# Optimization experiments

Measured on AMD Instinct MI355X. Metric: run time of the kernel, lower is better.

The kernel has to match this reference:

```python
import jax, jax.numpy as jnp
import numpy as np

B, S, D = 2, 1024, 512
NH, HD = 8, 64          # num_heads, head_dim
NS, F3 = 8, 1536        # shared experts, ffn_dim_shared = 3*D
E, F2 = 32, 1024        # routed experts, ffn_dim_routed = 2*D
R, K = 64, 4            # router_rank, num_activated_experts


def _ln(x, w, b, eps=1e-5):
    m = x.mean(-1, keepdims=True)
    v = ((x - m) ** 2).mean(-1, keepdims=True)
    return (x - m) * jax.lax.rsqrt(v + eps) * w + b


def _rms(x, w, eps=1e-6):
    return x * jax.lax.rsqrt((x * x).mean(-1, keepdims=True) + eps) * w


def _l2n(x, eps=1e-12):
    return x / jnp.maximum(jnp.linalg.norm(x, axis=-1, keepdims=True), eps)


def setup_inputs() -> dict:
    key = jax.random.key(0)
    ks = iter(jax.random.split(key, 40))
    sc = 0.02
    n = lambda shape: jax.random.normal(next(ks), shape, dtype=jnp.float32) * sc
    inp = {
        'x': jax.random.normal(next(ks), (B, S, D), dtype=jnp.float32),
        'ln1_w': jnp.ones((D,)), 'ln1_b': jnp.zeros((D,)),
        'ln2_w': jnp.ones((D,)), 'ln2_b': jnp.zeros((D,)),
        # per-head attention params, stacked over heads
        'q_w': n((NH, D, HD)), 'q_b': jnp.zeros((NH, HD)),
        'k_w': n((NH, D, HD)), 'k_b': jnp.zeros((NH, HD)),
        'v_w': n((NH, D, HD)), 'v_b': jnp.zeros((NH, HD)),
        'aw1': n((NH, D, HD // 2)), 'ab1': jnp.zeros((NH, HD // 2)),
        'aw2': n((NH, HD // 2, HD)), 'ab2': jnp.zeros((NH, HD)),
        'bw': n((NH, D, HD)), 'bb': jnp.zeros((NH, HD)),
        'scw1': n((NH, D, HD // 2)), 'scb1': jnp.zeros((NH, HD // 2)),
        'scw2': n((NH, HD // 2, HD)), 'scb2': jnp.zeros((NH, HD)),
        'arms_w': jnp.ones((NH, HD)),
        'l1_w': n((NH, HD, HD)), 'l1_b': jnp.zeros((NH, HD)),
        'out_w': n((D, D)), 'out_b': jnp.zeros((D,)),
        # MoE params
        'sh_rms': jnp.ones((NS, D)),
        'sh_w1': n((NS, D, F3)), 'sh_w2': n((NS, F3, D)), 'sh_w3': n((NS, D, F3)),
        'r_w1': n((E, D, F2)), 'r_w2': n((E, F2, D)), 'r_w3': n((E, D, F2)),
        'rd_w': n((D, R)), 'ru_w': n((R, E)),
    }
    return inp


def _forward(x, ln1_w, ln1_b, ln2_w, ln2_b, q_w, q_b, k_w, k_b, v_w, v_b,
             aw1, ab1, aw2, ab2, bw, bb, scw1, scb1, scw2, scb2, arms_w,
             l1_w, l1_b, out_w, out_b, sh_rms, sh_w1, sh_w2, sh_w3,
             r_w1, r_w2, r_w3, rd_w, ru_w):
    silu, sig = jax.nn.silu, jax.nn.sigmoid
    # ---- attention sublayer (dropout = identity in eval) ----
    residual = x
    xn = _ln(x, ln1_w, ln1_b)                                   # [B,S,D]
    q = _l2n(silu(jnp.einsum('bsd,hdk->bhsk', xn, q_w) + q_b[None, :, None, :]))
    k = _l2n(silu(jnp.einsum('bsd,hdk->bhsk', xn, k_w) + k_b[None, :, None, :]))
    v = silu(jnp.einsum('bsd,hdk->bhsk', xn, v_w) + v_b[None, :, None, :])
    alpha = sig(jnp.einsum('bhsr,hrk->bhsk',
                           jnp.einsum('bsd,hdr->bhsr', xn, aw1) + ab1[None, :, None, :],
                           aw2) + ab2[None, :, None, :])
    beta = sig(jnp.einsum('bsd,hdk->bhsk', xn, bw) + bb[None, :, None, :])
    shortcut = sig(jnp.einsum('bhsr,hrk->bhsk',
                              jnp.einsum('bsd,hdr->bhsr', xn, scw1) + scb1[None, :, None, :],
                              scw2) + scb2[None, :, None, :])
    v = v * alpha + beta
    scores = jnp.einsum('bhsk,bhtk->bhst', q, k) / jnp.sqrt(jnp.float32(HD))
    o = jnp.einsum('bhst,bhtk->bhsk', jax.nn.softmax(scores, axis=-1), v)
    o = _rms(o, arms_w[None, :, None, :]) * shortcut
    o = jnp.einsum('bhsk,hkj->bhsj', o, l1_w) + l1_b[None, :, None, :]
    o = o.transpose(0, 2, 1, 3).reshape(B, S, D)                # concat heads
    x = residual + (o @ out_w + out_b)
    # ---- MoE sublayer ----
    residual = x
    xf = _ln(x, ln2_w, ln2_b).reshape(-1, D)                    # [T,D]
    T = xf.shape[0]
    # shared experts (AdvancedExpert: rmsnorm -> swiglu -> +residual), averaged
    rb = xf * jax.lax.rsqrt((xf * xf).mean(-1, keepdims=True) + 1e-6)
    hn = rb[None] * sh_rms[:, None, :]                          # [NS,T,D]
    gate = silu(jnp.einsum('ntd,ndf->ntf', hn, sh_w1))
    val = jnp.einsum('ntd,ndf->ntf', hn, sh_w3)
    sh_out = jnp.einsum('ntf,nfd->ntd', gate * val, sh_w2) + xf[None]
    shared = sh_out.sum(0) / NS
    # router (low-rank) + top-k softmax weights
    logits = (xf @ rd_w) @ ru_w                                 # [T,E]
    top_v, top_i = jax.lax.top_k(logits, K)
    rw = jax.nn.softmax(top_v, axis=-1)                         # [T,K]
    w_full = jnp.zeros((T, E), xf.dtype).at[jnp.arange(T)[:, None], top_i].add(rw)
    # routed experts: dense compute, masked combine (same math)
    rg = silu(jnp.einsum('td,edf->etf', xf, r_w1))
    rv = jnp.einsum('td,edf->etf', xf, r_w3)
    eo = jnp.einsum('etf,efd->etd', rg * rv, r_w2)              # [E,T,D]
    routed = jnp.einsum('etd,te->td', eo, w_full)
    x = residual + (shared + routed).reshape(B, S, D)
    counts = jnp.zeros((E,), jnp.float32).at[top_i.reshape(-1)].add(1.0)
    load_balance_loss = jnp.var(counts, ddof=1)
    return x, load_balance_loss


def reference(x, ln1_w, ln1_b, ln2_w, ln2_b, q_w, q_b, k_w, k_b, v_w, v_b,
              aw1, ab1, aw2, ab2, bw, bb, scw1, scb1, scw2, scb2, arms_w,
              l1_w, l1_b, out_w, out_b, sh_rms, sh_w1, sh_w2, sh_w3,
              r_w1, r_w2, r_w3, rd_w, ru_w):
    return _forward(x, ln1_w, ln1_b, ln2_w, ln2_b, q_w, q_b, k_w, k_b, v_w, v_b,
                    aw1, ab1, aw2, ab2, bw, bb, scw1, scb1, scw2, scb2, arms_w,
                    l1_w, l1_b, out_w, out_b, sh_rms, sh_w1, sh_w2, sh_w3,
                    r_w1, r_w2, r_w3, rd_w, ru_w)
```

## Files before the change

kernel.cpp:

```cpp
#include <hip/hip_runtime.h>
#include <cmath>
#include <cstdint>


typedef __bf16 bf16;
typedef __bf16 bf16x8 __attribute__((ext_vector_type(8)));
typedef __bf16 bf16x4 __attribute__((ext_vector_type(4)));
typedef float  f32x4  __attribute__((ext_vector_type(4)));

static constexpr int Bb = 2, Ss = 1024, Dd = 512, NHh = 8, HDd = 64;
static constexpr int Tt = Bb * Ss;
static constexpr int NSs = 8, F3f = 1536;
static constexpr int Ee = 32, F2f = 1024;
static constexpr int SLOTCAP = 10240;
static constexpr int MAXTILE = 160;

__device__ inline float wavesum(float v) {
#pragma unroll
  for (int i = 1; i < 64; i <<= 1) v += __shfl_xor(v, i, 64);
  return v;
}
__device__ inline float blocksum(float v, float* sm) {
  v = wavesum(v);
  int wv = threadIdx.x >> 6;
// ... 96 lines not shown
    for (int r = 0; r < 4; ++r) {
      int grow = bm * 64 + wave * 16 + quad * 4 + r;
      float v;
      if (DUAL) {
        v = silu_f(acc0[nt][r]) * acc1[nt][r];
      } else {
        v = acc0[nt][r] * scale;
        if (bias) v += (float)bias[z * biasBatch + gcol];
        if (ACT == 1) v = silu_f(v);
        else if (ACT == 2) v = sigm_f(v);
      }
      if (RESID) v += (float)resid[(long)grow * resLd + gcol];
      long ci = (long)z * cBatch + (long)grow * ldc + gcol;
      if (ACCUM) atomicAdd((float*)Cv + ci, v);
      else if (OUTBF) ((bf16*)Cv)[ci] = (bf16)v;
      else ((float*)Cv)[ci] = v;
    }
  }
}

template <typename TI, int WANT, int SCALE>
__global__ __launch_bounds__(256) void tconv_k(
    const unsigned short* __restrict__ xdet,
    const TI* __restrict__ W, long wBatch,
    const TI* __restrict__ sc, long sBatch,
    bf16* __restrict__ Wt, long oBatch, int K, int N) {
  if (is_f32(xdet) != WANT) return;
  __shared__ float sT[64][65];
  const int tid = threadIdx.x;
  const int k0 = blockIdx.x * 64, n0 = blockIdx.y * 64, z = blockIdx.z;
  const TI* Wz = W + (long)z * wBatch;
  const int rr = tid >> 4, cc = (tid & 15) * 4;
#pragma unroll
  for (int it = 0; it < 4; ++it) {
    int row = it * 16 + rr;
    const TI* p = Wz + (long)(k0 + row) * N + n0 + cc;
    float v0, v1, v2, v3;
    if constexpr (sizeof(TI) == 4) {
      float4 v = *(const float4*)p;
      v0 = v.x; v1 = v.y; v2 = v.z; v3 = v.w;
    } else {
      bf16x4 v = *(const bf16x4*)p;
      v0 = (float)v[0]; v1 = (float)v[1]; v2 = (float)v[2]; v3 = (float)v[3];
    }
    if (SCALE) {
      float s = (float)sc[(long)z * sBatch + k0 + row];
      v0 *= s; v1 *= s; v2 *= s; v3 *= s;
    }
    sT[row][cc + 0] = v0; sT[row][cc + 1] = v1;
    sT[row][cc + 2] = v2; sT[row][cc + 3] = v3;
  }
  __syncthreads();
  bf16* Oz = Wt + (long)z * oBatch;
#pragma unroll
  for (int it = 0; it < 4; ++it) {
    int n = it * 16 + rr;
    bf16x4 ov;
#pragma unroll
    for (int j = 0; j < 4; ++j) ov[j] = (bf16)sT[cc + j][n];
    *(bf16x4*)(Oz + (long)(n0 + n) * K + k0 + cc) = ov;
  }
}

template <int DUAL, int ACCUM>
__global__ __launch_bounds__(256) void gemmT_k(
    const bf16* __restrict__ A, long aBatch, int lda,
    const bf16* __restrict__ B0t, const bf16* __restrict__ B1t, long bBatch,
    void* __restrict__ Cv, long cBatch, int ldc, int K, float scale) {
  __shared__ __align__(16) bf16 sA[128 * 40];
  __shared__ __align__(16) bf16 sB0[64 * 40];
  __shared__ __align__(16) bf16 sB1[DUAL ? 64 * 40 : 16];
  const int tid = threadIdx.x, wave = tid >> 6, lane = tid & 63;
  const int fm = lane & 15, quad = lane >> 4;
  const bf16* Az = A + (long)blockIdx.z * aBatch + (long)(blockIdx.x * 128) * lda;
  const bf16* B0z = B0t + (long)blockIdx.z * bBatch + (long)(blockIdx.y * 64) * K;
  const bf16* B1z = DUAL ? (B1t + (long)blockIdx.z * bBatch + (long)(blockIdx.y * 64) * K) : nullptr;
  f32x4 acc0[2][4], acc1[2][4];
  const f32x4 vz = {0.f, 0.f, 0.f, 0.f};
#pragma unroll
  for (int m = 0; m < 2; ++m)
#pragma unroll
    for (int n = 0; n < 4; ++n) { acc0[m][n] = vz; acc1[m][n] = vz; }
  const int srow = tid >> 2, sk0 = (tid & 3) * 8;
  for (int kb = 0; kb < K; kb += 32) {
    *(bf16x8*)(sA + srow * 40 + sk0) =
        *(const bf16x8*)(Az + (long)srow * lda + kb + sk0);
    *(bf16x8*)(sA + (srow + 64) * 40 + sk0) =
        *(const bf16x8*)(Az + (long)(srow + 64) * lda + kb + sk0);
    *(bf16x8*)(sB0 + srow * 40 + sk0) =
        *(const bf16x8*)(B0z + (long)srow * K + kb + sk0);
    if (DUAL)
      *(bf16x8*)(sB1 + srow * 40 + sk0) =
          *(const bf16x8*)(B1z + (long)srow * K + kb + sk0);
    __syncthreads();
    bf16x8 af0 = *(const bf16x8*)(sA + (wave * 32 + fm) * 40 + quad * 8);
    bf16x8 af1 = *(const bf16x8*)(sA + (wave * 32 + 16 + fm) * 40 + quad * 8);
#pragma unroll
    for (int nt = 0; nt < 4; ++nt) {
      bf16x8 b0 = *(const bf16x8*)(sB0 + (nt * 16 + fm) * 40 + quad * 8);
      acc0[0][nt] = __builtin_amdgcn_mfma_f32_16x16x32_bf16(af0, b0, acc0[0][nt], 0, 0, 0);
      acc0[1][nt] = __builtin_amdgcn_mfma_f32_16x16x32_bf16(af1, b0, acc0[1][nt], 0, 0, 0);
      if (DUAL) {
        bf16x8 b1 = *(const bf16x8*)(sB1 + (nt * 16 + fm) * 40 + quad * 8);
        acc1[0][nt] = __builtin_amdgcn_mfma_f32_16x16x32_bf16(af0, b1, acc1[0][nt], 0, 0, 0);
        acc1[1][nt] = __builtin_amdgcn_mfma_f32_16x16x32_bf16(af1, b1, acc1[1][nt], 0, 0, 0);
      }
    }
    __syncthreads();
  }
#pragma unroll
  for (int mt = 0; mt < 2; ++mt)
#pragma unroll
    for (int nt = 0; nt < 4; ++nt) {
      int col = blockIdx.y * 64 + nt * 16 + fm;
#pragma unroll
      for (int r = 0; r < 4; ++r) {
        int row = blockIdx.x * 128 + wave * 32 + mt * 16 + quad * 4 + r;
        long ci = (long)blockIdx.z * cBatch + (long)row * ldc + col;
        if (DUAL) {
          ((bf16*)Cv)[ci] = (bf16)(silu_f(acc0[mt][nt][r]) * acc1[mt][nt][r]);
        } else {
          float v = acc0[mt][nt][r] * scale;
          if (ACCUM) atomicAdd((float*)Cv + ci, v);
          else ((bf16*)Cv)[ci] = (bf16)v;
        }
      }
    }
}

__global__ __launch_bounds__(256) void moeT1_k(
    const int* __restrict__ tileExp, const int* __restrict__ tileStart,
    const int* __restrict__ slotTok, const bf16* __restrict__ xfb,
    const bf16* __restrict__ W1t, const bf16* __restrict__ W3t,
    bf16* __restrict__ hid) {
  int e = tileExp[blockIdx.x];
  if (e < 0) return;
  int slot0 = tileStart[blockIdx.x];
  __shared__ int sTok[64];
  __shared__ __align__(16) bf16 sA[64 * 40];
  __shared__ __align__(16) bf16 sB0[128 * 40];
  __shared__ __align__(16) bf16 sB1[128 * 40];
  const int tid = threadIdx.x, wave = tid >> 6, lane = tid & 63;
  const int fm = lane & 15, quad = lane >> 4;
  const int wr = wave >> 1, wc = wave & 1;
  if (tid < 64) sTok[tid] = slotTok[slot0 + tid];
  __syncthreads();
  const bf16* B0 = W1t + (long)e * (F2f * 512) + (long)(blockIdx.y * 128) * 512;
  const bf16* B1 = W3t + (long)e * (F2f * 512) + (long)(blockIdx.y * 128) * 512;
  f32x4 acc0[2][4], acc1[2][4];
  const f32x4 vz = {0.f, 0.f, 0.f, 0.f};
#pragma unroll
  for (int m = 0; m < 2; ++m)
#pragma unroll
    for (int n = 0; n < 4; ++n) { acc0[m][n] = vz; acc1[m][n] = vz; }
  const int srow = tid >> 2, sk0 = (tid & 3) * 8;
  const long atok = (long)sTok[srow] * 512;
  for (int kb = 0; kb < 512; kb += 32) {
    *(bf16x8*)(sA + srow * 40 + sk0) = *(const bf16x8*)(xfb + atok + kb + sk0);
    *(bf16x8*)(sB0 + srow * 40 + sk0) =
        *(const bf16x8*)(B0 + (long)srow * 512 + kb + sk0);
    *(bf16x8*)(sB0 + (srow + 64) * 40 + sk0) =
        *(const bf16x8*)(B0 + (long)(srow + 64) * 512 + kb + sk0);
    *(bf16x8*)(sB1 + srow * 40 + sk0) =
        *(const bf16x8*)(B1 + (long)srow * 512 + kb + sk0);
    *(bf16x8*)(sB1 + (srow + 64) * 40 + sk0) =
        *(const bf16x8*)(B1 + (long)(srow + 64) * 512 + kb + sk0);
    __syncthreads();
    bf16x8 af0 = *(const bf16x8*)(sA + (wr * 32 + fm) * 40 + quad * 8);
    bf16x8 af1 = *(const bf16x8*)(sA + (wr * 32 + 16 + fm) * 40 + quad * 8);
#pragma unroll
    for (int nt = 0; nt < 4; ++nt) {
      bf16x8 b0 = *(const bf16x8*)(sB0 + (wc * 64 + nt * 16 + fm) * 40 + quad * 8);
      acc0[0][nt] = __builtin_amdgcn_mfma_f32_16x16x32_bf16(af0, b0, acc0[0][nt], 0, 0, 0);
      acc0[1][nt] = __builtin_amdgcn_mfma_f32_16x16x32_bf16(af1, b0, acc0[1][nt], 0, 0, 0);
      bf16x8 b1 = *(const bf16x8*)(sB1 + (wc * 64 + nt * 16 + fm) * 40 + quad * 8);
      acc1[0][nt] = __builtin_amdgcn_mfma_f32_16x16x32_bf16(af0, b1, acc1[0][nt], 0, 0, 0);
      acc1[1][nt] = __builtin_amdgcn_mfma_f32_16x16x32_bf16(af1, b1, acc1[1][nt], 0, 0, 0);
    }
    __syncthreads();
  }
#pragma unroll
  for (int mt = 0; mt < 2; ++mt)
#pragma unroll
    for (int nt = 0; nt < 4; ++nt) {
      int col = blockIdx.y * 128 + wc * 64 + nt * 16 + fm;
#pragma unroll
      for (int r = 0; r < 4; ++r) {
        int row = wr * 32 + mt * 16 + quad * 4 + r;
        hid[(long)(slot0 + row) * F2f + col] =
            (bf16)(silu_f(acc0[mt][nt][r]) * acc1[mt][nt][r]);
      }
    }
}

__global__ __launch_bounds__(256) void moeT2_k(
    const int* __restrict__ tileExp, const int* __restrict__ tileStart,
    const int* __restrict__ slotTok, const float* __restrict__ slotW,
    const bf16* __restrict__ hid, const bf16* __restrict__ W2t,
    float* __restrict__ acc) {
  int e = tileExp[blockIdx.x];
  if (e < 0) return;
  int slot0 = tileStart[blockIdx.x];
  __shared__ int sTok[64];
  __shared__ float sW[64];
  __shared__ __align__(16) bf16 sA[64 * 40];
  __shared__ __align__(16) bf16 sB[128 * 40];
  const int tid = threadIdx.x, wave = tid >> 6, lane = tid & 63;
  const int fm = lane & 15, quad = lane >> 4;
  const int wr = wave >> 1, wc = wave & 1;
  if (tid < 64) { sTok[tid] = slotTok[slot0 + tid]; sW[tid] = slotW[slot0 + tid]; }
  __syncthreads();
  const bf16* B = W2t + (long)e * (512 * F2f) + (long)(blockIdx.y * 128) * F2f;
  f32x4 acc0[2][4];
  const f32x4 vz = {0.f, 0.f, 0.f, 0.f};
#pragma unroll
  for (int m = 0; m < 2; ++m)
#pragma unroll
    for (int n = 0; n < 4; ++n) acc0[m][n] = vz;
  const int srow = tid >> 2, sk0 = (tid & 3) * 8;
  for (int kb = 0; kb < F2f; kb += 32) {
    *(bf16x8*)(sA + srow * 40 + sk0) =
        *(const bf16x8*)(hid + (long)(slot0 + srow) * F2f + kb + sk0);
    *(bf16x8*)(sB + srow * 40 + sk0) =
        *(const bf16x8*)(B + (long)srow * F2f + kb + sk0);
    *(bf16x8*)(sB + (srow + 64) * 40 + sk0) =
        *(const bf16x8*)(B + (long)(srow + 64) * F2f + kb + sk0);
    __syncthreads();
    bf16x8 af0 = *(const bf16x8*)(sA + (wr * 32 + fm) * 40 + quad * 8);
    bf16x8 af1 = *(const bf16x8*)(sA + (wr * 32 + 16 + fm) * 40 + quad * 8);
#pragma unroll
    for (int nt = 0; nt < 4; ++nt) {
      bf16x8 b0 = *(const bf16x8*)(sB + (wc * 64 + nt * 16 + fm) * 40 + quad * 8);
      acc0[0][nt] = __builtin_amdgcn_mfma_f32_16x16x32_bf16(af0, b0, acc0[0][nt], 0, 0, 0);
      acc0[1][nt] = __builtin_amdgcn_mfma_f32_16x16x32_bf16(af1, b0, acc0[1][nt], 0, 0, 0);
    }
    __syncthreads();
  }
#pragma unroll
  for (int mt = 0; mt < 2; ++mt)
#pragma unroll
    for (int nt = 0; nt < 4; ++nt) {
      int col = blockIdx.y * 128 + wc * 64 + nt * 16 + fm;
#pragma unroll
      for (int r = 0; r < 4; ++r) {
        int row = wr * 32 + mt * 16 + quad * 4 + r;
        atomicAdd(acc + (long)sTok[row] * 512 + col, acc0[mt][nt][r] * sW[row]);
      }
    }
}

template <typename TB, int WANT>
__global__ __launch_bounds__(256) void moe1_k(
    const unsigned short* __restrict__ xdet,
    const int* __restrict__ tileExp, const int* __restrict__ tileStart,
    const int* __restrict__ slotTok,
    const bf16* __restrict__ xfb,
    const TB* __restrict__ W1, const TB* __restrict__ W3,
    bf16* __restrict__ hid, int Ps, int colOff, int Np) {
  if (is_f32(xdet) != WANT) return;
  int e = tileExp[blockIdx.x];
  if (e < 0) return;
  int slot0 = tileStart[blockIdx.x];
  __shared__ int sTok[64];
  __shared__ __align__(16) bf16 sA[64 * 40];
  __shared__ __align__(16) bf16 sB0[64 * 40];
  __shared__ __align__(16) bf16 sB1[64 * 40];
  const int tid = threadIdx.x;
  const int wave = tid >> 6, lane = tid & 63;
  const int fm = lane & 15, quad = lane >> 4;
  if (tid < 64) sTok[tid] = slotTok[slot0 + tid];
  __syncthreads();
  const TB* B0 = W1 + (long)e * 512 * F2f + colOff;
  const TB* B1 = W3 + (long)e * 512 * F2f + colOff;
  const int bn = blockIdx.y;
  f32x4 acc0[4], acc1[4];
  const f32x4 vz = {0.f, 0.f, 0.f, 0.f};
#pragma unroll
  for (int i = 0; i < 4; ++i) { acc0[i] = vz; acc1[i] = vz; }
  const int arow = tid >> 2, ak0 = (tid & 3) * 8;
  const int gn = bn * 64 + lane;
  const int wch = wave * 8;
  for (int kb = 0; kb < 512; kb += 32) {
    int tok = sTok[arow];
    *(bf16x8*)(sA + arow * 40 + ak0) =
        *(const bf16x8*)(xfb + (long)tok * 512 + kb + ak0);
    bf16x8 bv, cv;
    if (gn < Np) {
      const TB* bp = B0 + (long)(kb + wch) * F2f + gn;
      const TB* cp = B1 + (long)(kb + wch) * F2f + gn;
#pragma unroll
      for (int j = 0; j < 8; ++j) {
        bv[j] = (bf16)(float)bp[(long)j * F2f];
        cv[j] = (bf16)(float)cp[(long)j * F2f];
      }
    } else {
#pragma unroll
      for (int j = 0; j < 8; ++j) { bv[j] = (bf16)0.f; cv[j] = (bf16)0.f; }
    }
    *(bf16x8*)(sB0 + lane * 40 + wch) = bv;
    *(bf16x8*)(sB1 + lane * 40 + wch) = cv;
    __syncthreads();
    bf16x8 af = *(const bf16x8*)(sA + (wave * 16 + fm) * 40 + quad * 8);
#pragma unroll
    for (int nt = 0; nt < 4; ++nt) {
      bf16x8 bfr = *(const bf16x8*)(sB0 + (nt * 16 + fm) * 40 + quad * 8);
      acc0[nt] = __builtin_amdgcn_mfma_f32_16x16x32_bf16(af, bfr, acc0[nt], 0, 0, 0);
      bf16x8 bg = *(const bf16x8*)(sB1 + (nt * 16 + fm) * 40 + quad * 8);
      acc1[nt] = __builtin_amdgcn_mfma_f32_16x16x32_bf16(af, bg, acc1[nt], 0, 0, 0);
    }
    __syncthreads();
  }
#pragma unroll
  for (int nt = 0; nt < 4; ++nt) {
    int gcol = bn * 64 + nt * 16 + fm;
    if (gcol >= Np) continue;
#pragma unroll
    for (int r = 0; r < 4; ++r) {
      int row = wave * 16 + quad * 4 + r;
      hid[(long)(slot0 + row) * Ps + gcol] =
          (bf16)(silu_f(acc0[nt][r]) * acc1[nt][r]);
    }
  }
}

template <typename TB, int WANT>
__global__ __launch_bounds__(256) void moe2_k(
    const unsigned short* __restrict__ xdet,
    const int* __restrict__ tileExp, const int* __restrict__ tileStart,
    const int* __restrict__ slotTok, const float* __restrict__ slotW,
// ... 234 lines not shown
  float ms = wavesum(ov * ov) * (1.f / 64.f);
  float s = rsqrtf(ms + 1e-6f);
  o[i] = (bf16)(ov * s * (float)arms[h * 64 + lane] * (float)sc[i]);
}

template <typename T, int WANT>
__global__ __launch_bounds__(256) void router_k(const unsigned short* __restrict__ xdet,
                                                const float* __restrict__ x2,
                                                const T* __restrict__ lnw,
                                                const T* __restrict__ lnb,
                                                const T* __restrict__ rdw,
                                                const T* __restrict__ ruw,
                                                int* __restrict__ eidx,
                                                float* __restrict__ ew,
                                                int* __restrict__ counts) {
  if (is_f32(xdet) != WANT) return;
  __shared__ float sx[4][512];
  __shared__ float st[4][64];
  __shared__ float sl[4][32];
  int wv = threadIdx.x >> 6, lane = threadIdx.x & 63;
  long t = (long)blockIdx.x * 4 + wv;
  float v[8];
  float s1 = 0.f;
#pragma unroll
  for (int j = 0; j < 8; ++j) { v[j] = x2[t * 512 + lane * 8 + j]; s1 += v[j]; }
  float mean = wavesum(s1) * (1.f / 512.f);
  float s2 = 0.f;
#pragma unroll
  for (int j = 0; j < 8; ++j) { float d = v[j] - mean; s2 += d * d; }
  float rv = rsqrtf(wavesum(s2) * (1.f / 512.f) + 1e-5f);
#pragma unroll
  for (int j = 0; j < 8; ++j)
    sx[wv][lane * 8 + j] = (v[j] - mean) * rv * (float)lnw[lane * 8 + j] + (float)lnb[lane * 8 + j];
  __syncthreads();
  float acc = 0.f;
  for (int d = 0; d < 512; ++d) acc += sx[wv][d] * (float)rdw[d * 64 + lane];
  st[wv][lane] = acc;
  __syncthreads();
  if (lane < 32) {
    float lg = 0.f;
    for (int r = 0; r < 64; ++r) lg += st[wv][r] * (float)ruw[r * 32 + lane];
    sl[wv][lane] = lg;
  }
  __syncthreads();
  if (lane == 0) {
    float vv[32];
#pragma unroll
    for (int e = 0; e < 32; ++e) vv[e] = sl[wv][e];
    int idx[4]; float tv[4];
#pragma unroll
    for (int k = 0; k < 4; ++k) {
      float best = -1e30f; int bi = 0;
      for (int e = 0; e < 32; ++e)
        if (vv[e] > best) { best = vv[e]; bi = e; }
      tv[k] = best; idx[k] = bi; vv[bi] = -1e30f;
    }
    float m = tv[0], s = 0.f, w[4];
#pragma unroll
    for (int k = 0; k < 4; ++k) { w[k] = expf(tv[k] - m); s += w[k]; }
    float inv = 1.f / s;
#pragma unroll
    for (int k = 0; k < 4; ++k) {
      eidx[t * 4 + k] = idx[k];
      ew[t * 4 + k] = w[k] * inv;
      atomicAdd(&counts[idx[k]], 1);
    }
  }
}

__global__ void offsets_k(const int* __restrict__ counts, int* __restrict__ segOff,
                          int* __restrict__ tileExp, int* __restrict__ tileStart) {
  if (threadIdx.x != 0) return;
  int off = 0, ti = 0;
  for (int e = 0; e < Ee; ++e) {
    segOff[e] = off;
    int pc = (counts[e] + 63) & ~63;
    for (int i = 0; i < pc / 64; ++i) { tileExp[ti] = e; tileStart[ti] = off + i * 64; ++ti; }
    off += pc;
  }
  for (; ti < 192; ++ti) tileExp[ti] = -1;
}
__global__ void scatter_k(const int* __restrict__ eidx, const float* __restrict__ ew,
                          const int* __restrict__ segOff, int* __restrict__ cursor,
                          int* __restrict__ slotTok, float* __restrict__ slotW) {
  int t = blockIdx.x * 256 + threadIdx.x;
#pragma unroll
  for (int k = 0; k < 4; ++k) {
    int e = eidx[t * 4 + k];
    int pos = atomicAdd(&cursor[e], 1);
    int s = segOff[e] + pos;
    slotTok[s] = t;
    slotW[s] = ew[t * 4 + k];
  }
}
__global__ void pad_k(const int* __restrict__ counts, const int* __restrict__ segOff,
                      int* __restrict__ slotTok, float* __restrict__ slotW) {
  int e = blockIdx.x;
  int c = counts[e], pc = (c + 63) & ~63;
  for (int i = c + threadIdx.x; i < pc; i += 64) {
    int s = segOff[e] + i;
    slotTok[s] = 0;
    slotW[s] = 0.f;
  }
}

__global__ void zero_k(float* __restrict__ p, long n) {
  long i = (long)blockIdx.x * blockDim.x + threadIdx.x;
  long st = (long)gridDim.x * blockDim.x;
  for (; i < n; i += st) p[i] = 0.f;
}
template <typename TW, typename TO, int WANT>
__global__ __launch_bounds__(256) void final_k(const unsigned short* __restrict__ xdet,
                                               const float* __restrict__ x2,
                                               const TW* __restrict__ lnw,
                                               const TW* __restrict__ lnb,
                                               const float* __restrict__ acc,
                                               TO* __restrict__ out) {
  if (is_f32(xdet) != WANT) return;
  __shared__ float sm[4];
  long base = (long)blockIdx.x * 512;
  int tid = threadIdx.x;
  float x0 = x2[base + tid], x1 = x2[base + 256 + tid];
  float mean = blocksum(x0 + x1, sm) * (1.f / 512.f);
  float d0 = x0 - mean, d1 = x1 - mean;
  float var = blocksum(d0 * d0 + d1 * d1, sm) * (1.f / 512.f);
  float r = rsqrtf(var + 1e-5f);
  float f0 = d0 * r * (float)lnw[tid] + (float)lnb[tid];
  float f1 = d1 * r * (float)lnw[256 + tid] + (float)lnb[256 + tid];
  out[base + tid] = (TO)(x0 + f0 + acc[base + tid]);
  out[base + 256 + tid] = (TO)(x1 + f1 + acc[base + 256 + tid]);
}
template <typename TO, int WANT>
__global__ void loss_k(const unsigned short* __restrict__ xdet,
                       const int* __restrict__ counts, TO* __restrict__ out) {
  if (is_f32(xdet) != WANT) return;
  int lane = threadIdx.x;
  float c = lane < 32 ? (float)counts[lane] : 0.f;
  float mean = wavesum(c) * (1.f / 32.f);
  float d = lane < 32 ? (c - mean) * (c - mean) : 0.f;
  float var = wavesum(d) * (1.f / 31.f);
  if (lane == 0) out[(long)Tt * 512] = (TO)var;
}

template <int ACT, int DUAL, int OUTBF, int ACCUM, int RESID, int ASCALE>
static inline void G(dim3 grid, hipStream_t st, const unsigned short* xdet,
                     const bf16* A, long aB, int lda,
                     const void* ascale, long asOff, long asB,
                     const void* B0, long b0Off, const void* B1, long b1Off,
                     long bB, int bK,
                     const void* bias, int biasB,
                     void* C, long cB, int ldc,
                     const void* resid, int resLd,
                     int N, int K, float scale) {
  gemm_k<float, 1, ACT, DUAL, OUTBF, ACCUM, RESID, ASCALE><<<grid, 256, 0, st>>>(
      xdet, A, aB, lda,
      ascale ? (const float*)ascale + asOff : nullptr, asB,
      (const float*)B0 + b0Off, B1 ? (const float*)B1 + b1Off : nullptr, bB, bK,
      bias ? (const float*)bias : nullptr, biasB, C, cB, ldc,
      resid ? (const float*)resid : nullptr, resLd, N, K, scale);
  gemm_k<bf16, 0, ACT, DUAL, OUTBF, ACCUM, RESID, ASCALE><<<grid, 256, 0, st>>>(
      xdet, A, aB, lda,
      ascale ? (const bf16*)ascale + asOff : nullptr, asB,
      (const bf16*)B0 + b0Off, B1 ? (const bf16*)B1 + b1Off : nullptr, bB, bK,
      bias ? (const bf16*)bias : nullptr, biasB, C, cB, ldc,
      resid ? (const bf16*)resid : nullptr, resLd, N, K, scale);
}

template <int SC>
static inline void CVT(hipStream_t st, const unsigned short* xdet, const void* W,
                       const void* sc, bf16* Wt, int K, int N, int batch,
                       long wB, long sB, long oB) {
  dim3 g(K / 64, N / 64, batch);
  tconv_k<float, 1, SC><<<g, 256, 0, st>>>(xdet, (const float*)W, wB,
                                           (const float*)sc, sB, Wt, oB, K, N);
  tconv_k<bf16, 0, SC><<<g, 256, 0, st>>>(xdet, (const bf16*)W, wB,
                                          (const bf16*)sc, sB, Wt, oB, K, N);
}

extern "C" void kernel_launch(void* const* d_in, const int* in_sizes, int n_in,
                              void* d_out, int out_size, void* d_ws, size_t ws_size,
                              hipStream_t stream) {
  (void)in_sizes; (void)n_in; (void)out_size;
  const void* x    = d_in[0];
  const void* ln1w = d_in[1];
  const void* ln1b = d_in[2];
  const void* ln2w = d_in[3];
  const void* ln2b = d_in[4];
  const void* q_w  = d_in[5];
  const void* q_b  = d_in[6];
  const void* k_w  = d_in[7];
  const void* k_b  = d_in[8];
  const void* v_w  = d_in[9];
  const void* v_b  = d_in[10];
  const void* aw1  = d_in[11];
  const void* ab1  = d_in[12];
  const void* aw2  = d_in[13];
  const void* ab2  = d_in[14];
  const void* bw   = d_in[15];
  const void* bbv  = d_in[16];
  const void* scw1 = d_in[17];
  const void* scb1 = d_in[18];
  const void* scw2 = d_in[19];
  const void* scb2 = d_in[20];
  const void* arms = d_in[21];
  const void* l1w  = d_in[22];
  const void* l1b  = d_in[23];
  const void* outw = d_in[24];
  const void* outb = d_in[25];
  const void* shrms= d_in[26];
  const void* shw1 = d_in[27];
  const void* shw2 = d_in[28];
  const void* shw3 = d_in[29];
  const void* rw1  = d_in[30];
  const void* rw2  = d_in[31];
  const void* rw3  = d_in[32];
  const void* rdw  = d_in[33];
  const void* ruw  = d_in[34];
  const unsigned short* xdet = (const unsigned short*)x;

  constexpr size_t MB = 1u << 20;
  char* base = (char*)d_ws;
  bf16* xn    = (bf16*)(base + 0 * MB);
  bf16* qh    = (bf16*)(base + 2 * MB);
  bf16* kh    = (bf16*)(base + 4 * MB);
  bf16* vh    = (bf16*)(base + 6 * MB);
  bf16* beta  = (bf16*)(base + 8 * MB);
  bf16* ah    = (bf16*)(base + 10 * MB);
  bf16* alpha = (bf16*)(base + 12 * MB);
  bf16* sch   = (bf16*)(base + 8 * MB);
  bf16* shct  = (bf16*)(base + 14 * MB);
  bf16* oatt  = (bf16*)(base + 8 * MB);
  bf16* conc  = (bf16*)(base + 2 * MB);
  float* x2   = (float*)(base + 4 * MB);
  bf16* xfb   = (bf16*)(base + 0 * MB);
  bf16* rbb   = (bf16*)(base + 2 * MB);
  float* acc  = (float*)(base + 12 * MB);
  int*   hcnt = (int*)(base + 8 * MB);
  int*   hcur = hcnt + 32;
  int*   hseg = hcnt + 64;
  int*   hte  = hcnt + 96;
  int*   hts  = hcnt + 288;
  int*   heidx= hcnt + 512;
  float* hew  = (float*)(hcnt + 512 + 8192);
  int*   hstok= hcnt + 512 + 16384;
  float* hsw  = (float*)(hcnt + 512 + 16384 + 10240);

  size_t rem = ws_size > (size_t)16 * MB ? ws_size - (size_t)16 * MB : 0;
  const size_t SH1B  = (size_t)NSs * F3f * Dd * 2;
  const size_t R1B   = (size_t)Ee * F2f * Dd * 2;
  const size_t HIDRT = (size_t)SLOTCAP * F2f * 2;
  const size_t HID1  = (size_t)Tt * F3f * 2;
  const bool cvtRt = rem >= 3 * SH1B + 3 * R1B + HIDRT;
  const bool cvtSh = cvtRt || rem >= 3 * SH1B + HID1;
  char* cur = base + (size_t)16 * MB;
  bf16 *sh1t = nullptr, *sh3t = nullptr, *sh2t = nullptr;
  bf16 *r1t = nullptr, *r3t = nullptr, *r2t = nullptr;
  if (cvtSh) {
    sh1t = (bf16*)cur; cur += SH1B;
    sh3t = (bf16*)cur; cur += SH1B;
    sh2t = (bf16*)cur; cur += SH1B;
  }
  if (cvtRt) {
    r1t = (bf16*)cur; cur += R1B;
    r3t = (bf16*)cur; cur += R1B;
    r2t = (bf16*)cur; cur += R1B;
  }
  bf16* hid; long hidElems;
  if (ws_size >= 20 * MB) {
    hid = (bf16*)cur;
    hidElems = (long)((base + ws_size) - cur) / 2;
  } else {
    hid = (bf16*)(base + 8 * MB + 256 * 1024);
    hidElems = (long)(4 * MB - 256 * 1024) / 2;
  }

  ln_k<float, float, 1><<<Tt, 256, 0, stream>>>(xdet, (const float*)x, (const float*)ln1w, (const float*)ln1b, xn, 1e-5f);
  ln_k<bf16, bf16, 0><<<Tt, 256, 0, stream>>>(xdet, (const bf16*)x, (const bf16*)ln1w, (const bf16*)ln1b, xn, 1e-5f);

  G<1,0,1,0,0,0>(dim3(32,1,8), stream, xdet, xn,0,512, nullptr,0,0, q_w,0,nullptr,0,(long)512*64,64, q_b,64, qh,(long)Tt*64,64, nullptr,0, 64,512,1.f);
  G<1,0,1,0,0,0>(dim3(32,1,8), stream, xdet, xn,0,512, nullptr,0,0, k_w,0,nullptr,0,(long)512*64,64, k_b,64, kh,(long)Tt*64,64, nullptr,0, 64,512,1.f);
  G<1,0,1,0,0,0>(dim3(32,1,8), stream, xdet, xn,0,512, nullptr,0,0, v_w,0,nullptr,0,(long)512*64,64, v_b,64, vh,(long)Tt*64,64, nullptr,0, 64,512,1.f);
  G<2,0,1,0,0,0>(dim3(32,1,8), stream, xdet, xn,0,512, nullptr,0,0, bw,0,nullptr,0,(long)512*64,64, bbv,64, beta,(long)Tt*64,64, nullptr,0, 64,512,1.f);
  G<0,0,1,0,0,0>(dim3(32,1,8), stream, xdet, xn,0,512, nullptr,0,0, aw1,0,nullptr,0,(long)512*32,32, ab1,32, ah,(long)Tt*32,32, nullptr,0, 32,512,1.f);
  G<2,0,1,0,0,0>(dim3(32,1,8), stream, xdet, ah,(long)Tt*32,32, nullptr,0,0, aw2,0,nullptr,0,(long)32*64,64, ab2,64, alpha,(long)Tt*64,64, nullptr,0, 64,32,1.f);

  postproj_k<<<NHh * Tt / 4, 256, 0, stream>>>(qh, kh, vh, alpha, beta);

  G<0,0,1,0,0,0>(dim3(32,1,8), stream, xdet, xn,0,512, nullptr,0,0, scw1,0,nullptr,0,(long)512*32,32, scb1,32, sch,(long)Tt*32,32, nullptr,0, 32,512,1.f);
  G<2,0,1,0,0,0>(dim3(32,1,8), stream, xdet, sch,(long)Tt*32,32, nullptr,0,0, scw2,0,nullptr,0,(long)32*64,64, scb2,64, shct,(long)Tt*64,64, nullptr,0, 64,32,1.f);

  attn_k<<<dim3(16, 16), 256, 0, stream>>>(qh, kh, vh, oatt);

  orms_k<float, 1><<<NHh * Tt / 4, 256, 0, stream>>>(xdet, oatt, (const float*)arms, shct);
  orms_k<bf16, 0><<<NHh * Tt / 4, 256, 0, stream>>>(xdet, oatt, (const bf16*)arms, shct);

  G<0,0,1,0,0,0>(dim3(32,1,8), stream, xdet, oatt,(long)Tt*64,64, nullptr,0,0, l1w,0,nullptr,0,(long)64*64,64, l1b,64, conc,64,512, nullptr,0, 64,64,1.f);
  G<0,0,0,0,1,0>(dim3(32,8,1), stream, xdet, conc,0,512, nullptr,0,0, outw,0,nullptr,0,0,512, outb,0, x2,0,512, x,512, 512,512,1.f);

  ln_k<float, float, 1><<<Tt, 256, 0, stream>>>(xdet, x2, (const float*)ln2w, (const float*)ln2b, xfb, 1e-5f);
  ln_k<float, bf16, 0><<<Tt, 256, 0, stream>>>(xdet, x2, (const bf16*)ln2w, (const bf16*)ln2b, xfb, 1e-5f);
  rms_k<<<Tt, 256, 0, stream>>>(xfb, rbb);
  zero_k<<<256, 256, 0, stream>>>(acc, (long)Tt * 512);
  zero_k<<<1, 64, 0, stream>>>((float*)hcnt, 64);
  router_k<float, 1><<<Tt / 4, 256, 0, stream>>>(xdet, x2, (const float*)ln2w, (const float*)ln2b, (const float*)rdw, (const float*)ruw, heidx, hew, hcnt);
  router_k<bf16, 0><<<Tt / 4, 256, 0, stream>>>(xdet, x2, (const bf16*)ln2w, (const bf16*)ln2b, (const bf16*)rdw, (const bf16*)ruw, heidx, hew, hcnt);
  offsets_k<<<1, 64, 0, stream>>>(hcnt, hseg, hte, hts);
  scatter_k<<<Tt / 256, 256, 0, stream>>>(heidx, hew, hseg, hcur, hstok, hsw);
  pad_k<<<Ee, 64, 0, stream>>>(hcnt, hseg, hstok, hsw);

  if (cvtSh) {
    CVT<1>(stream, xdet, shw1, shrms, sh1t, 512, F3f, NSs, (long)512*F3f, 512, (long)F3f*512);
    CVT<1>(stream, xdet, shw3, shrms, sh3t, 512, F3f, NSs, (long)512*F3f, 512, (long)F3f*512);
    CVT<0>(stream, xdet, shw2, nullptr, sh2t, F3f, 512, NSs, (long)F3f*512, 0, (long)512*F3f);
  }
  if (cvtRt) {
    CVT<0>(stream, xdet, rw1, nullptr, r1t, 512, F2f, Ee, (long)512*F2f, 0, (long)F2f*512);
    CVT<0>(stream, xdet, rw3, nullptr, r3t, 512, F2f, Ee, (long)512*F2f, 0, (long)F2f*512);
    CVT<0>(stream, xdet, rw2, nullptr, r2t, F2f, 512, Ee, (long)F2f*512, 0, (long)512*F2f);
  }

  if (cvtSh) {
    int zB = (int)((hidElems * 2) / (long)HID1);
    if (zB > NSs) zB = NSs;
    if (zB < 1) zB = 1;
    for (int e0 = 0; e0 < NSs; e0 += zB) {
      int zc = NSs - e0 < zB ? NSs - e0 : zB;
      gemmT_k<1, 0><<<dim3(Tt / 128, F3f / 64, zc), 256, 0, stream>>>(
          rbb, 0, 512, sh1t + (long)e0 * F3f * 512, sh3t + (long)e0 * F3f * 512,
          (long)F3f * 512, hid, (long)Tt * F3f, F3f, 512, 1.f);
      gemmT_k<0, 1><<<dim3(Tt / 128, 512 / 64, zc), 256, 0, stream>>>(
          hid, (long)Tt * F3f, F3f, sh2t + (long)e0 * 512 * F3f, nullptr,
          (long)512 * F3f, acc, 0, 512, F3f, 0.125f);
    }
  } else {
    int PsS, zBsh;
    if (hidElems >= (long)Tt * F3f) {
      PsS = F3f;
      zBsh = (int)(hidElems / ((long)Tt * F3f)); if (zBsh > NSs) zBsh = NSs;
    } else {
      PsS = (int)((hidElems / Tt / 32) * 32); if (PsS > F3f) PsS = F3f;
      zBsh = 1;
    }
    for (int n0e = 0; n0e < NSs; n0e += zBsh) {
      int zc = NSs - n0e < zBsh ? NSs - n0e : zBsh;
      for (int off = 0; off < F3f; off += PsS) {
        int Np = F3f - off < PsS ? F3f - off : PsS;
        G<0,1,1,0,0,1>(dim3(32,(Np+63)/64,zc), stream, xdet, rbb,0,512,
                       shrms,(long)n0e*512,512,
                       shw1,(long)n0e*512*F3f + off, shw3,(long)n0e*512*F3f + off,
                       (long)512*F3f, F3f,
                       nullptr,0, hid,(long)Tt*PsS,PsS, nullptr,0, Np,512,1.f);
        G<0,0,0,1,0,0>(dim3(32,8,zc), stream, xdet, hid,(long)Tt*PsS,PsS, nullptr,0,0,
                       shw2,(long)n0e*F3f*512 + (long)off*512, nullptr,0,
                       (long)F3f*512, 512,
                       nullptr,0, acc,0,512, nullptr,0, 512,Np,0.125f);
      }
    }
  }

  if (cvtRt) {
    moeT1_k<<<dim3(MAXTILE, F2f / 128), 256, 0, stream>>>(hte, hts, hstok, xfb, r1t, r3t, hid);
    moeT2_k<<<dim3(MAXTILE, 512 / 128), 256, 0, stream>>>(hte, hts, hstok, hsw, hid, r2t, acc);
  } else {
    int PsR = (int)((hidElems / SLOTCAP / 32) * 32);
    if (PsR > F2f) PsR = F2f;
    if (PsR < 32) PsR = 32;
    for (int off = 0; off < F2f; off += PsR) {
      int Np = F2f - off < PsR ? F2f - off : PsR;
      dim3 g1(MAXTILE, (Np + 63) / 64);
      moe1_k<float, 1><<<g1, 256, 0, stream>>>(xdet, hte, hts, hstok, xfb, (const float*)rw1, (const float*)rw3, hid, PsR, off, Np);
      moe1_k<bf16, 0><<<g1, 256, 0, stream>>>(xdet, hte, hts, hstok, xfb, (const bf16*)rw1, (const bf16*)rw3, hid, PsR, off, Np);
      dim3 g2(MAXTILE, 8);
      moe2_k<float, 1><<<g2, 256, 0, stream>>>(xdet, hte, hts, hstok, hsw, hid, PsR, off, Np, (const float*)rw2, acc);
      moe2_k<bf16, 0><<<g2, 256, 0, stream>>>(xdet, hte, hts, hstok, hsw, hid, PsR, off, Np, (const bf16*)rw2, acc);
    }
  }

  final_k<float, float, 1><<<Tt, 256, 0, stream>>>(xdet, x2, (const float*)ln2w, (const float*)ln2b, acc, (float*)d_out);
  final_k<bf16, bf16, 0><<<Tt, 256, 0, stream>>>(xdet, x2, (const bf16*)ln2w, (const bf16*)ln2b, acc, (bf16*)d_out);
  loss_k<float, 1><<<1, 64, 0, stream>>>(xdet, hcnt, (float*)d_out);
  loss_k<bf16, 0><<<1, 64, 0, stream>>>(xdet, hcnt, (bf16*)d_out);
}
```

Before: 1.113 ms.

## Prefetch GEMM tiles into registers and replace atomic combine with gather reduction

```diff
diff --git a/kernel.cpp b/kernel.cpp
--- a/kernel.cpp
+++ b/kernel.cpp
@@ -202,17 +202,26 @@
 #pragma unroll
     for (int n = 0; n < 4; ++n) { acc0[m][n] = vz; acc1[m][n] = vz; }
   const int srow = tid >> 2, sk0 = (tid & 3) * 8;
+  const bf16* Ap0 = Az + (long)srow * lda + sk0;
+  const bf16* Ap1 = Az + (long)(srow + 64) * lda + sk0;
+  const bf16* Bp0 = B0z + (long)srow * K + sk0;
+  const bf16* Bp1 = DUAL ? (B1z + (long)srow * K + sk0) : Bp0;
+  bf16x8 rA0 = *(const bf16x8*)(Ap0);
+  bf16x8 rA1 = *(const bf16x8*)(Ap1);
+  bf16x8 rB0 = *(const bf16x8*)(Bp0);
+  bf16x8 rB1 = rB0;
+  if (DUAL) rB1 = *(const bf16x8*)(Bp1);
   for (int kb = 0; kb < K; kb += 32) {
-    *(bf16x8*)(sA + srow * 40 + sk0) =
-        *(const bf16x8*)(Az + (long)srow * lda + kb + sk0);
-    *(bf16x8*)(sA + (srow + 64) * 40 + sk0) =
-        *(const bf16x8*)(Az + (long)(srow + 64) * lda + kb + sk0);
-    *(bf16x8*)(sB0 + srow * 40 + sk0) =
-        *(const bf16x8*)(B0z + (long)srow * K + kb + sk0);
-    if (DUAL)
-      *(bf16x8*)(sB1 + srow * 40 + sk0) =
-          *(const bf16x8*)(B1z + (long)srow * K + kb + sk0);
-    __syncthreads();
+    *(bf16x8*)(sA + srow * 40 + sk0) = rA0;
+    *(bf16x8*)(sA + (srow + 64) * 40 + sk0) = rA1;
+    *(bf16x8*)(sB0 + srow * 40 + sk0) = rB0;
+    if (DUAL) *(bf16x8*)(sB1 + srow * 40 + sk0) = rB1;
+    __syncthreads();
+    int kn = kb + 32 < K ? kb + 32 : kb;
+    rA0 = *(const bf16x8*)(Ap0 + kn);
+    rA1 = *(const bf16x8*)(Ap1 + kn);
+    rB0 = *(const bf16x8*)(Bp0 + kn);
+    if (DUAL) rB1 = *(const bf16x8*)(Bp1 + kn);
     bf16x8 af0 = *(const bf16x8*)(sA + (wave * 32 + fm) * 40 + quad * 8);
     bf16x8 af1 = *(const bf16x8*)(sA + (wave * 32 + 16 + fm) * 40 + quad * 8);
 #pragma unroll
@@ -241,7 +250,8 @@
           ((bf16*)Cv)[ci] = (bf16)(silu_f(acc0[mt][nt][r]) * acc1[mt][nt][r]);
         } else {
           float v = acc0[mt][nt][r] * scale;
-          if (ACCUM) atomicAdd((float*)Cv + ci, v);
+          if (ACCUM == 1) atomicAdd((float*)Cv + ci, v);
+          else if (ACCUM == 2) ((float*)Cv)[ci] = v;
           else ((bf16*)Cv)[ci] = (bf16)v;
         }
       }
@@ -274,18 +284,29 @@
 #pragma unroll
     for (int n = 0; n < 4; ++n) { acc0[m][n] = vz; acc1[m][n] = vz; }
   const int srow = tid >> 2, sk0 = (tid & 3) * 8;
-  const long atok = (long)sTok[srow] * 512;
+  const bf16* Ap  = xfb + (long)sTok[srow] * 512 + sk0;
+  const bf16* B0p = B0 + (long)srow * 512 + sk0;
+  const bf16* B0q = B0 + (long)(srow + 64) * 512 + sk0;
+  const bf16* B1p = B1 + (long)srow * 512 + sk0;
+  const bf16* B1q = B1 + (long)(srow + 64) * 512 + sk0;
+  bf16x8 rA  = *(const bf16x8*)(Ap);
+  bf16x8 rB0 = *(const bf16x8*)(B0p);
+  bf16x8 rB1 = *(const bf16x8*)(B0q);
+  bf16x8 rB2 = *(const bf16x8*)(B1p);
+  bf16x8 rB3 = *(const bf16x8*)(B1q);
   for (int kb = 0; kb < 512; kb += 32) {
-    *(bf16x8*)(sA + srow * 40 + sk0) = *(const bf16x8*)(xfb + atok + kb + sk0);
-    *(bf16x8*)(sB0 + srow * 40 + sk0) =
-        *(const bf16x8*)(B0 + (long)srow * 512 + kb + sk0);
-    *(bf16x8*)(sB0 + (srow + 64) * 40 + sk0) =
-        *(const bf16x8*)(B0 + (long)(srow + 64) * 512 + kb + sk0);
-    *(bf16x8*)(sB1 + srow * 40 + sk0) =
-        *(const bf16x8*)(B1 + (long)srow * 512 + kb + sk0);
-    *(bf16x8*)(sB1 + (srow + 64) * 40 + sk0) =
-        *(const bf16x8*)(B1 + (long)(srow + 64) * 512 + kb + sk0);
-    __syncthreads();
+    *(bf16x8*)(sA + srow * 40 + sk0) = rA;
+    *(bf16x8*)(sB0 + srow * 40 + sk0) = rB0;
+    *(bf16x8*)(sB0 + (srow + 64) * 40 + sk0) = rB1;
+    *(bf16x8*)(sB1 + srow * 40 + sk0) = rB2;
+    *(bf16x8*)(sB1 + (srow + 64) * 40 + sk0) = rB3;
+    __syncthreads();
+    int kn = kb + 32 < 512 ? kb + 32 : kb;
+    rA  = *(const bf16x8*)(Ap + kn);
+    rB0 = *(const bf16x8*)(B0p + kn);
+    rB1 = *(const bf16x8*)(B0q + kn);
+    rB2 = *(const bf16x8*)(B1p + kn);
+    rB3 = *(const bf16x8*)(B1q + kn);
     bf16x8 af0 = *(const bf16x8*)(sA + (wr * 32 + fm) * 40 + quad * 8);
     bf16x8 af1 = *(const bf16x8*)(sA + (wr * 32 + 16 + fm) * 40 + quad * 8);
 #pragma unroll
@@ -313,11 +334,12 @@
     }
 }
 
+template <int GATHER>
 __global__ __launch_bounds__(256) void moeT2_k(
     const int* __restrict__ tileExp, const int* __restrict__ tileStart,
     const int* __restrict__ slotTok, const float* __restrict__ slotW,
     const bf16* __restrict__ hid, const bf16* __restrict__ W2t,
-    float* __restrict__ acc) {
+    float* __restrict__ acc, float* __restrict__ eoRt) {
   int e = tileExp[blockIdx.x];
   if (e < 0) return;
   int slot0 = tileStart[blockIdx.x];
@@ -329,7 +351,6 @@
   const int fm = lane & 15, quad = lane >> 4;
   const int wr = wave >> 1, wc = wave & 1;
   if (tid < 64) { sTok[tid] = slotTok[slot0 + tid]; sW[tid] = slotW[slot0 + tid]; }
-  __syncthreads();
   const bf16* B = W2t + (long)e * (512 * F2f) + (long)(blockIdx.y * 128) * F2f;
   f32x4 acc0[2][4];
   const f32x4 vz = {0.f, 0.f, 0.f, 0.f};
@@ -338,14 +359,21 @@
 #pragma unroll
     for (int n = 0; n < 4; ++n) acc0[m][n] = vz;
   const int srow = tid >> 2, sk0 = (tid & 3) * 8;
+  const bf16* Ap  = hid + (long)(slot0 + srow) * F2f + sk0;
+  const bf16* Bp0 = B + (long)srow * F2f + sk0;
+  const bf16* Bp1 = B + (long)(srow + 64) * F2f + sk0;
+  bf16x8 rA  = *(const bf16x8*)(Ap);
+  bf16x8 rB0 = *(const bf16x8*)(Bp0);
+  bf16x8 rB1 = *(const bf16x8*)(Bp1);
   for (int kb = 0; kb < F2f; kb += 32) {
-    *(bf16x8*)(sA + srow * 40 + sk0) =
-        *(const bf16x8*)(hid + (long)(slot0 + srow) * F2f + kb + sk0);
-    *(bf16x8*)(sB + srow * 40 + sk0) =
-        *(const bf16x8*)(B + (long)srow * F2f + kb + sk0);
-    *(bf16x8*)(sB + (srow + 64) * 40 + sk0) =
-        *(const bf16x8*)(B + (long)(srow + 64) * F2f + kb + sk0);
-    __syncthreads();
+    *(bf16x8*)(sA + srow * 40 + sk0) = rA;
+    *(bf16x8*)(sB + srow * 40 + sk0) = rB0;
+    *(bf16x8*)(sB + (srow + 64) * 40 + sk0) = rB1;
+    __syncthreads();
+    int kn = kb + 32 < F2f ? kb + 32 : kb;
+    rA  = *(const bf16x8*)(Ap + kn);
+    rB0 = *(const bf16x8*)(Bp0 + kn);
+    rB1 = *(const bf16x8*)(Bp1 + kn);
     bf16x8 af0 = *(const bf16x8*)(sA + (wr * 32 + fm) * 40 + quad * 8);
     bf16x8 af1 = *(const bf16x8*)(sA + (wr * 32 + 16 + fm) * 40 + quad * 8);
 #pragma unroll
@@ -364,7 +392,11 @@
 #pragma unroll
       for (int r = 0; r < 4; ++r) {
         int row = wr * 32 + mt * 16 + quad * 4 + r;
-        atomicAdd(acc + (long)sTok[row] * 512 + col, acc0[mt][nt][r] * sW[row]);
+        if (GATHER) {
+          eoRt[(long)(slot0 + row) * 512 + col] = acc0[mt][nt][r] * sW[row];
+        } else {
+          atomicAdd(acc + (long)sTok[row] * 512 + col, acc0[mt][nt][r] * sW[row]);
+        }
       }
     }
 }
@@ -765,7 +797,8 @@
 }
 __global__ void scatter_k(const int* __restrict__ eidx, const float* __restrict__ ew,
                           const int* __restrict__ segOff, int* __restrict__ cursor,
-                          int* __restrict__ slotTok, float* __restrict__ slotW) {
+                          int* __restrict__ slotTok, float* __restrict__ slotW,
+                          int* __restrict__ slotOf) {
   int t = blockIdx.x * 256 + threadIdx.x;
 #pragma unroll
   for (int k = 0; k < 4; ++k) {
@@ -774,6 +807,7 @@
     int s = segOff[e] + pos;
     slotTok[s] = t;
     slotW[s] = ew[t * 4 + k];
+    slotOf[t * 4 + k] = s;
   }
 }
 __global__ void pad_k(const int* __restrict__ counts, const int* __restrict__ segOff,
@@ -798,6 +832,9 @@
                                                const TW* __restrict__ lnw,
                                                const TW* __restrict__ lnb,
                                                const float* __restrict__ acc,
+                                               const float* __restrict__ eoSh,
+                                               const float* __restrict__ eoRt,
+                                               const int* __restrict__ slotOf,
                                                TO* __restrict__ out) {
   if (is_f32(xdet) != WANT) return;
   __shared__ float sm[4];
@@ -810,8 +847,26 @@
   float r = rsqrtf(var + 1e-5f);
   float f0 = d0 * r * (float)lnw[tid] + (float)lnb[tid];
   float f1 = d1 * r * (float)lnw[256 + tid] + (float)lnb[256 + tid];
-  out[base + tid] = (TO)(x0 + f0 + acc[base + tid]);
-  out[base + 256 + tid] = (TO)(x1 + f1 + acc[base + 256 + tid]);
+  float a0 = 0.f, a1 = 0.f;
+  if (acc) { a0 = acc[base + tid]; a1 = acc[base + 256 + tid]; }
+  if (eoSh) {
+#pragma unroll
+    for (int e2 = 0; e2 < NSs; ++e2) {
+      a0 += eoSh[(long)e2 * Tt * 512 + base + tid];
+      a1 += eoSh[(long)e2 * Tt * 512 + base + 256 + tid];
+    }
+  }
+  if (eoRt) {
+    long t = blockIdx.x;
+#pragma unroll
+    for (int k2 = 0; k2 < 4; ++k2) {
+      long s = slotOf[t * 4 + k2];
+      a0 += eoRt[s * 512 + tid];
+      a1 += eoRt[s * 512 + 256 + tid];
+    }
+  }
+  out[base + tid] = (TO)(x0 + f0 + a0);
+  out[base + 256 + tid] = (TO)(x1 + f1 + a1);
 }
 template <typename TO, int WANT>
 __global__ void loss_k(const unsigned short* __restrict__ xdet,
@@ -927,26 +982,41 @@
   float* hew  = (float*)(hcnt + 512 + 8192);
   int*   hstok= hcnt + 512 + 16384;
   float* hsw  = (float*)(hcnt + 512 + 16384 + 10240);
+  int*   hslot= hcnt + 512 + 16384 + 20480;
 
   size_t rem = ws_size > (size_t)16 * MB ? ws_size - (size_t)16 * MB : 0;
   const size_t SH1B  = (size_t)NSs * F3f * Dd * 2;
   const size_t R1B   = (size_t)Ee * F2f * Dd * 2;
   const size_t HIDRT = (size_t)SLOTCAP * F2f * 2;
   const size_t HID1  = (size_t)Tt * F3f * 2;
+  const size_t EORT  = (size_t)SLOTCAP * 512 * 4;
+  const size_t EOSH  = (size_t)NSs * Tt * 512 * 4;
   const bool cvtRt = rem >= 3 * SH1B + 3 * R1B + HIDRT;
   const bool cvtSh = cvtRt || rem >= 3 * SH1B + HID1;
   char* cur = base + (size_t)16 * MB;
   bf16 *sh1t = nullptr, *sh3t = nullptr, *sh2t = nullptr;
   bf16 *r1t = nullptr, *r3t = nullptr, *r2t = nullptr;
+  size_t used = 0;
   if (cvtSh) {
     sh1t = (bf16*)cur; cur += SH1B;
     sh3t = (bf16*)cur; cur += SH1B;
     sh2t = (bf16*)cur; cur += SH1B;
+    used += 3 * SH1B;
   }
   if (cvtRt) {
     r1t = (bf16*)cur; cur += R1B;
     r3t = (bf16*)cur; cur += R1B;
     r2t = (bf16*)cur; cur += R1B;
+    used += 3 * R1B;
+  }
+  bool gather = false;
+  float* eoRt = nullptr;
+  float* eoSh = nullptr;
+  if (cvtRt && rem - used >= EORT + HIDRT) {
+    eoRt = (float*)cur; cur += EORT; used += EORT; gather = true;
+  }
+  if (gather && rem - used >= EOSH + HIDRT) {
+    eoSh = (float*)cur; cur += EOSH; used += EOSH;
   }
   bf16* hid; long hidElems;
   if (ws_size >= 20 * MB) {
@@ -956,6 +1026,7 @@
     hid = (bf16*)(base + 8 * MB + 256 * 1024);
     hidElems = (long)(4 * MB - 256 * 1024) / 2;
   }
+  const bool accUsed = (eoSh == nullptr) || !gather;
 
   ln_k<float, float, 1><<<Tt, 256, 0, stream>>>(xdet, (const float*)x, (const float*)ln1w, (const float*)ln1b, xn, 1e-5f);
   ln_k<bf16, bf16, 0><<<Tt, 256, 0, stream>>>(xdet, (const bf16*)x, (const bf16*)ln1w, (const bf16*)ln1b, xn, 1e-5f);
@@ -983,12 +1054,12 @@
   ln_k<float, float, 1><<<Tt, 256, 0, stream>>>(xdet, x2, (const float*)ln2w, (const float*)ln2b, xfb, 1e-5f);
   ln_k<float, bf16, 0><<<Tt, 256, 0, stream>>>(xdet, x2, (const bf16*)ln2w, (const bf16*)ln2b, xfb, 1e-5f);
   rms_k<<<Tt, 256, 0, stream>>>(xfb, rbb);
-  zero_k<<<256, 256, 0, stream>>>(acc, (long)Tt * 512);
+  if (accUsed) zero_k<<<256, 256, 0, stream>>>(acc, (long)Tt * 512);
   zero_k<<<1, 64, 0, stream>>>((float*)hcnt, 64);
   router_k<float, 1><<<Tt / 4, 256, 0, stream>>>(xdet, x2, (const float*)ln2w, (const float*)ln2b, (const float*)rdw, (const float*)ruw, heidx, hew, hcnt);
   router_k<bf16, 0><<<Tt / 4, 256, 0, stream>>>(xdet, x2, (const bf16*)ln2w, (const bf16*)ln2b, (const bf16*)rdw, (const bf16*)ruw, heidx, hew, hcnt);
   offsets_k<<<1, 64, 0, stream>>>(hcnt, hseg, hte, hts);
-  scatter_k<<<Tt / 256, 256, 0, stream>>>(heidx, hew, hseg, hcur, hstok, hsw);
+  scatter_k<<<Tt / 256, 256, 0, stream>>>(heidx, hew, hseg, hcur, hstok, hsw, hslot);
   pad_k<<<Ee, 64, 0, stream>>>(hcnt, hseg, hstok, hsw);
 
   if (cvtSh) {
@@ -1003,7 +1074,7 @@
   }
 
   if (cvtSh) {
-    int zB = (int)((hidElems * 2) / (long)HID1);
+    int zB = (int)(((size_t)hidElems * 2) / HID1);
     if (zB > NSs) zB = NSs;
     if (zB < 1) zB = 1;
     for (int e0 = 0; e0 < NSs; e0 += zB) {
@@ -1011,9 +1082,16 @@
       gemmT_k<1, 0><<<dim3(Tt / 128, F3f / 64, zc), 256, 0, stream>>>(
           rbb, 0, 512, sh1t + (long)e0 * F3f * 512, sh3t + (long)e0 * F3f * 512,
           (long)F3f * 512, hid, (long)Tt * F3f, F3f, 512, 1.f);
-      gemmT_k<0, 1><<<dim3(Tt / 128, 512 / 64, zc), 256, 0, stream>>>(
-          hid, (long)Tt * F3f, F3f, sh2t + (long)e0 * 512 * F3f, nullptr,
-          (long)512 * F3f, acc, 0, 512, F3f, 0.125f);
+      if (eoSh) {
+        gemmT_k<0, 2><<<dim3(Tt / 128, 512 / 64, zc), 256, 0, stream>>>(
+            hid, (long)Tt * F3f, F3f, sh2t + (long)e0 * 512 * F3f, nullptr,
+            (long)512 * F3f, eoSh + (long)e0 * Tt * 512, (long)Tt * 512, 512,
+            F3f, 0.125f);
+      } else {
+        gemmT_k<0, 1><<<dim3(Tt / 128, 512 / 64, zc), 256, 0, stream>>>(
+            hid, (long)Tt * F3f, F3f, sh2t + (long)e0 * 512 * F3f, nullptr,
+            (long)512 * F3f, acc, 0, 512, F3f, 0.125f);
+      }
     }
   } else {
     int PsS, zBsh;
@@ -1043,7 +1121,11 @@
 
   if (cvtRt) {
     moeT1_k<<<dim3(MAXTILE, F2f / 128), 256, 0, stream>>>(hte, hts, hstok, xfb, r1t, r3t, hid);
-    moeT2_k<<<dim3(MAXTILE, 512 / 128), 256, 0, stream>>>(hte, hts, hstok, hsw, hid, r2t, acc);
+    if (gather) {
+      moeT2_k<1><<<dim3(MAXTILE, 512 / 128), 256, 0, stream>>>(hte, hts, hstok, hsw, hid, r2t, acc, eoRt);
+    } else {
+      moeT2_k<0><<<dim3(MAXTILE, 512 / 128), 256, 0, stream>>>(hte, hts, hstok, hsw, hid, r2t, acc, nullptr);
+    }
   } else {
     int PsR = (int)((hidElems / SLOTCAP / 32) * 32);
     if (PsR > F2f) PsR = F2f;
@@ -1059,8 +1141,10 @@
     }
   }
 
-  final_k<float, float, 1><<<Tt, 256, 0, stream>>>(xdet, x2, (const float*)ln2w, (const float*)ln2b, acc, (float*)d_out);
-  final_k<bf16, bf16, 0><<<Tt, 256, 0, stream>>>(xdet, x2, (const bf16*)ln2w, (const bf16*)ln2b, acc, (bf16*)d_out);
+  const float* accP = accUsed ? acc : nullptr;
+  const float* eoRtP = gather ? eoRt : nullptr;
+  final_k<float, float, 1><<<Tt, 256, 0, stream>>>(xdet, x2, (const float*)ln2w, (const float*)ln2b, accP, eoSh, eoRtP, hslot, (float*)d_out);
+  final_k<bf16, bf16, 0><<<Tt, 256, 0, stream>>>(xdet, x2, (const bf16*)ln2w, (const bf16*)ln2b, accP, eoSh, eoRtP, hslot, (bf16*)d_out);
   loss_k<float, 1><<<1, 64, 0, stream>>>(xdet, hcnt, (float*)d_out);
   loss_k<bf16, 0><<<1, 64, 0, stream>>>(xdet, hcnt, (bf16*)d_out);
 }
```

Measured after the change: 999.3 us. 1.11x faster.
